# Kernel tuning notes

Hardware: AMD Instinct MI355X
Metric: run time of the kernel (lower is better)

Reference implementation:

```python
import jax, jax.numpy as jnp
import numpy as np

ALPHA = 0.2  # LeakyReLU negative slope
NEG_INF = -9e15


def setup_inputs() -> dict:
    key = jax.random.key(0)
    ks = jax.random.split(key, 6)
    N, IN, OUT, E = 2048, 256, 256, 64
    inp = {
        "input": jax.random.normal(ks[0], (N, IN), dtype=jnp.float32),
        "adj": jax.random.randint(ks[1], (N, N), 0, 2, dtype=jnp.int32),
        "e_feat": jax.random.normal(ks[2], (N, N, E), dtype=jnp.float32),
        # xavier-uniform-like scale for params
        "W_e": jax.random.normal(ks[3], (E, IN), dtype=jnp.float32) * (1.414 * np.sqrt(2.0 / (E + IN))),
        "W": jax.random.normal(ks[4], (IN, OUT), dtype=jnp.float32) * (1.414 * np.sqrt(2.0 / (IN + OUT))),
        "a": jax.random.normal(ks[5], (3 * OUT, 1), dtype=jnp.float32) * (1.414 * np.sqrt(2.0 / (3 * OUT + 1))),
    }
    return inp


def reference(input, adj, e_feat, W_e, W, a):
    F = W.shape[1]
    # Decompose attention vector: cat([h_i, h_j, e_ij]) @ a == h_i@a1 + h_j@a2 + e_ij@a3
    a1, a2, a3 = a[:F, 0], a[F:2 * F, 0], a[2 * F:, 0]
    h = input @ W                              # [N, F]
    s_src = h @ a1                             # [N]
    s_dst = h @ a2                             # [N]
    # e_ij @ a3 where e = e_feat @ W_e @ W, folded by associativity into one [N,N] result
    s_edge = e_feat @ (W_e @ (W @ a3))         # [N, N]
    scores = jax.nn.leaky_relu(s_src[:, None] + s_dst[None, :] + s_edge, negative_slope=ALPHA)
    att = jnp.where(adj > 0, scores, NEG_INF)
    att = jax.nn.softmax(att, axis=1)
    h_prime = att @ h                          # [N, F]
    return jax.nn.elu(h_prime)                 # concat=True -> ELU
```

## Files before the change

kernel.cpp:

```cpp
#include <hip/hip_runtime.h>
#include <math.h>

#define NN   2048
#define INF_ 256
#define OUTF 256
#define EF   64
#define ALPHA 0.2f
#define NEG_INF -9000000000000000.0f

typedef unsigned short ushortT;
typedef __attribute__((ext_vector_type(8))) short    short8v;
typedef __attribute__((ext_vector_type(4))) short    short4v;
typedef __attribute__((ext_vector_type(8))) unsigned short u16x8;
typedef __attribute__((ext_vector_type(4))) float    f32x4;

__device__ __forceinline__ float b2f(ushortT u) {
    unsigned v = (unsigned)u << 16;
    return *(float*)&v;
}
__device__ __forceinline__ ushortT f2b(float f) {
    unsigned b = *(unsigned*)&f;
    unsigned r = (b + 0x7FFFu + ((b >> 16) & 1u)) >> 16;
    return (ushortT)r;
}
__device__ __forceinline__ float dpp_add_xor1(float x) {
    int xi = *(int*)&x;
    int r = __builtin_amdgcn_mov_dpp(xi, 0xB1, 0xF, 0xF, true);
    float rf = *(float*)&r;
    return x + rf;
}
__device__ __forceinline__ float dpp_add_xor2(float x) {
    int xi = *(int*)&x;
    int r = __builtin_amdgcn_mov_dpp(xi, 0x4E, 0xF, 0xF, true);
    float rf = *(float*)&r;
    return x + rf;
}

__global__ void prep1_kernel(const float* __restrict__ W, const float* __restrict__ a,
                             float* __restrict__ w3) {
    int lane = threadIdx.x & 63, wave = threadIdx.x >> 6;
    const float* a3 = a + 2 * OUTF;
    float4 av = *(const float4*)&a3[lane * 4];
    int r0 = blockIdx.x * 8 + wave * 2;
    #pragma unroll
    for (int rr = 0; rr < 2; ++rr) {
        int r = r0 + rr;
        float4 wv = *(const float4*)&W[(size_t)r * OUTF + lane * 4];
        float d = wv.x * av.x + wv.y * av.y + wv.z * av.z + wv.w * av.w;
        #pragma unroll
        for (int off = 32; off; off >>= 1) d += __shfl_xor(d, off);
        if (lane == 0) w3[r] = d;
    }
}

__global__ void prep2_kernel(const float* __restrict__ W_e, const float* __restrict__ w3,
                             float* __restrict__ we3) {
    int lane = threadIdx.x & 63, wave = threadIdx.x >> 6;
    int r = blockIdx.x * 4 + wave;
    float4 wv = *(const float4*)&W_e[(size_t)r * INF_ + lane * 4];
    float4 xv = *(const float4*)&w3[lane * 4];
    float d = wv.x * xv.x + wv.y * xv.y + wv.z * xv.z + wv.w * xv.w;
    #pragma unroll
    for (int off = 32; off; off >>= 1) d += __shfl_xor(d, off);
    if (lane == 0) we3[r] = d;
}

__global__ void sv_kernel(const float* __restrict__ h, const float* __restrict__ a,
                          float* __restrict__ s_src, float* __restrict__ s_dst) {
    int lane = threadIdx.x & 63;
    int wave = threadIdx.x >> 6;
    int i = blockIdx.x * 4 + wave;
    float acc1 = 0.f, acc2 = 0.f;
    #pragma unroll
    for (int u = 0; u < 4; ++u) {
        int o = lane + u * 64;
        float hv = h[(size_t)i * OUTF + o];
        acc1 += hv * a[o];
        acc2 += hv * a[OUTF + o];
    }
    #pragma unroll
    for (int off = 32; off; off >>= 1) {
        acc1 += __shfl_xor(acc1, off);
        acc2 += __shfl_xor(acc2, off);
    }
    if (lane == 0) { s_src[i] = acc1; s_dst[i] = acc2; }
}

template<int K>
__launch_bounds__(256, 2)
__global__ void gemm_kernel(const float* __restrict__ A, const float* __restrict__ Bm,
                            float* __restrict__ C) {
    __shared__ float As[64][68];
    __shared__ float Bs[64][32];
    int tid = threadIdx.x;
    int r0 = blockIdx.x * 64;
    int c0 = blockIdx.y * 32;
    int tr = tid >> 4;
    int tc = tid & 15;
    float acc[4][2] = {};

    for (int k0 = 0; k0 < K; k0 += 64) {
        #pragma unroll
        for (int t = 0; t < 4; ++t) {
            int s = tid + t * 256;
            int row = s >> 4, col4 = s & 15;
            *(float4*)&As[row][col4 * 4] =
                *(const float4*)&A[(size_t)(r0 + row) * K + k0 + col4 * 4];
        }
        #pragma unroll
        for (int t = 0; t < 2; ++t) {
            int s = tid + t * 256;
            int row = s >> 3, col4 = s & 7;
            *(float4*)&Bs[row][col4 * 4] =
                *(const float4*)&Bm[(size_t)(k0 + row) * 256 + c0 + col4 * 4];
        }
        __syncthreads();
        #pragma unroll
        for (int kk = 0; kk < 64; kk += 4) {
            float4 aReg[4];
            float2 bReg[4];
            #pragma unroll
            for (int i = 0; i < 4; ++i) aReg[i] = *(const float4*)&As[tr * 4 + i][kk];
            #pragma unroll
            for (int q = 0; q < 4; ++q)  bReg[q] = *(const float2*)&Bs[kk + q][tc * 2];
            #pragma unroll
            for (int q = 0; q < 4; ++q) {
                float bx = bReg[q].x, by = bReg[q].y;
                #pragma unroll
                for (int i = 0; i < 4; ++i) {
                    float av = (q == 0) ? aReg[i].x : (q == 1) ? aReg[i].y
                             : (q == 2) ? aReg[i].z : aReg[i].w;
                    acc[i][0] += av * bx;
                    acc[i][1] += av * by;
                }
            }
        }
        __syncthreads();
    }
    #pragma unroll
    for (int i = 0; i < 4; ++i) {
        int r = r0 + tr * 4 + i;
        float2 v = {acc[i][0], acc[i][1]};
        *(float2*)&C[(size_t)r * 256 + c0 + tc * 2] = v;
    }
}

__global__ void xpose_kernel(const float* __restrict__ h, ushortT* __restrict__ hbT) {
    __shared__ ushortT tb[64][72];
    int t = threadIdx.x;
    int r0 = blockIdx.x * 64;
    int n0 = blockIdx.y * 64;
    int row = t >> 2, seg = t & 3;
    #pragma unroll
    for (int c = 0; c < 4; ++c) {
        float4 v = *(const float4*)&h[(size_t)(r0 + row) * OUTF + n0 + seg * 16 + c * 4];
        tb[seg * 16 + c * 4 + 0][row] = f2b(v.x);
        tb[seg * 16 + c * 4 + 1][row] = f2b(v.y);
        tb[seg * 16 + c * 4 + 2][row] = f2b(v.z);
        tb[seg * 16 + c * 4 + 3][row] = f2b(v.w);
    }
    __syncthreads();
    *(u16x8*)&hbT[(size_t)(n0 + row) * NN + r0 + seg * 16] =
        *(const u16x8*)&tb[row][seg * 16];
    *(u16x8*)&hbT[(size_t)(n0 + row) * NN + r0 + seg * 16 + 8] =
        *(const u16x8*)&tb[row][seg * 16 + 8];
}

__launch_bounds__(256, 2)
__global__ void gemm2_mfma_kernel(const ushortT* __restrict__ attb,
                                  const ushortT* __restrict__ hbT,
                                  float* __restrict__ Cpart) {
    __shared__ ushortT As[64][72];
    __shared__ ushortT Bs[64][72];
    int tid = threadIdx.x;
    int lane = tid & 63;
    int w = tid >> 6;
    int r0 = blockIdx.x * 64;
    int c0 = blockIdx.y * 64;
    int z  = blockIdx.z;
    int m = lane & 15, q = lane >> 4;
    const int srow = tid >> 2, sseg = tid & 3;

    f32x4 acc0 = {0.f, 0.f, 0.f, 0.f};
    f32x4 acc1 = {0.f, 0.f, 0.f, 0.f};
    f32x4 acc2 = {0.f, 0.f, 0.f, 0.f};
    f32x4 acc3 = {0.f, 0.f, 0.f, 0.f};

    for (int k0 = z * (NN / 4); k0 < (z + 1) * (NN / 4); k0 += 64) {
        {
            const size_t abase = (size_t)(r0 + srow) * NN + k0 + sseg * 16;
            *(u16x8*)&As[srow][sseg * 16]     = *(const u16x8*)&attb[abase];
            *(u16x8*)&As[srow][sseg * 16 + 8] = *(const u16x8*)&attb[abase + 8];
            const size_t bbase = (size_t)(c0 + srow) * NN + k0 + sseg * 16;
            *(u16x8*)&Bs[srow][sseg * 16]     = *(const u16x8*)&hbT[bbase];
            *(u16x8*)&Bs[srow][sseg * 16 + 8] = *(const u16x8*)&hbT[bbase + 8];
        }
        __syncthreads();
        #pragma unroll
        for (int kk = 0; kk < 2; ++kk) {
            short4v a0 = *(const short4v*)&As[w * 16 + m][kk * 32 + q * 4];
            short4v a1 = *(const short4v*)&As[w * 16 + m][kk * 32 + 16 + q * 4];
            short8v af = {a0.x, a0.y, a0.z, a0.w, a1.x, a1.y, a1.z, a1.w};
            #pragma unroll
            for (int nb = 0; nb < 4; ++nb) {
                short4v b0 = *(const short4v*)&Bs[nb * 16 + m][kk * 32 + q * 4];
                short4v b1 = *(const short4v*)&Bs[nb * 16 + m][kk * 32 + 16 + q * 4];
                short8v bf = {b0.x, b0.y, b0.z, b0.w, b1.x, b1.y, b1.z, b1.w};
                if (nb == 0) acc0 = __builtin_amdgcn_mfma_f32_16x16x32_bf16(af, bf, acc0, 0, 0, 0);
                if (nb == 1) acc1 = __builtin_amdgcn_mfma_f32_16x16x32_bf16(af, bf, acc1, 0, 0, 0);
                if (nb == 2) acc2 = __builtin_amdgcn_mfma_f32_16x16x32_bf16(af, bf, acc2, 0, 0, 0);
                if (nb == 3) acc3 = __builtin_amdgcn_mfma_f32_16x16x32_bf16(af, bf, acc3, 0, 0, 0);
            }
        }
        __syncthreads();
    }
    float* Cz = Cpart + (size_t)z * NN * OUTF;
    #pragma unroll
    for (int r = 0; r < 4; ++r) {
        int row = r0 + w * 16 + q * 4 + r;
        Cz[(size_t)row * OUTF + c0 + 0  + m] = acc0[r];
        Cz[(size_t)row * OUTF + c0 + 16 + m] = acc1[r];
        Cz[(size_t)row * OUTF + c0 + 32 + m] = acc2[r];
        Cz[(size_t)row * OUTF + c0 + 48 + m] = acc3[r];
    }
}

__global__ void combine_kernel(const float* __restrict__ Cpart, const float* __restrict__ invs,
                               float* __restrict__ out) {
    int i = blockIdx.x, t = threadIdx.x;
    size_t idx = (size_t)i * OUTF + t;
    const size_t P = (size_t)NN * OUTF;
    float v = (Cpart[idx] + Cpart[P + idx] + Cpart[2 * P + idx] + Cpart[3 * P + idx]) * invs[i];
    out[idx] = v > 0.f ? v : __expf(v) - 1.f;
}

__launch_bounds__(256, 6)
__global__ void score_kernel(const float* __restrict__ e_feat, const int* __restrict__ adj,
                             const float* __restrict__ s_src, const float* __restrict__ s_dst,
                             const float* __restrict__ we3,
                             ushortT* __restrict__ attb, float* __restrict__ invs) {
    __shared__ float p[NN];
    __shared__ float sdst[NN];
    __shared__ unsigned char amask[NN];
    __shared__ float swe3[EF];
    __shared__ float redm[4], reds[4];

    int tid  = threadIdx.x;
    int lane = tid & 63;
    int wave = tid >> 6;
    int i    = blockIdx.x;

    const int* arow = adj + (size_t)i * NN;
    #pragma unroll
    for (int t = 0; t < 2; ++t) {
        int s = tid * 2 + t;
        int4 a4 = ((const int4*)arow)[s];
        uchar4 m4;
        m4.x = a4.x != 0; m4.y = a4.y != 0; m4.z = a4.z != 0; m4.w = a4.w != 0;
        *(uchar4*)&amask[s * 4] = m4;
        ((float4*)sdst)[s] = ((const float4*)s_dst)[s];
    }
    if (tid < EF) swe3[tid] = we3[tid];
    __syncthreads();

    const int g  = lane >> 2;
    const int gl = lane & 3;
    const float4 wv0 = *(const float4*)&swe3[0  + gl * 4];
    const float4 wv1 = *(const float4*)&swe3[16 + gl * 4];
    const float4 wv2 = *(const float4*)&swe3[32 + gl * 4];
    const float4 wv3 = *(const float4*)&swe3[48 + gl * 4];
    const float* efrow = e_feat + (size_t)i * NN * EF;
    const int joff = wave * 16 + g;

    unsigned mbits = 0;
    #pragma unroll
    for (int k = 0; k < 32; ++k)
        mbits |= (unsigned)(amask[k * 64 + joff] != 0) << k;

    #pragma unroll 4
    for (int k = 0; k < 32; ++k) {
        int j = k * 64 + joff;
        bool av = (mbits >> k) & 1u;
        float4 e0, e1, e2, e3;
        if (av) {
            const float* ep = efrow + (size_t)j * EF;
            e0 = *(const float4*)&ep[0  + gl * 4];
            e1 = *(const float4*)&ep[16 + gl * 4];
            e2 = *(const float4*)&ep[32 + gl * 4];
            e3 = *(const float4*)&ep[48 + gl * 4];
        }
        if (av) {
            float d = e0.x * wv0.x + e0.y * wv0.y + e0.z * wv0.z + e0.w * wv0.w
                    + e1.x * wv1.x + e1.y * wv1.y + e1.z * wv1.z + e1.w * wv1.w
                    + e2.x * wv2.x + e2.y * wv2.y + e2.z * wv2.z + e2.w * wv2.w
                    + e3.x * wv3.x + e3.y * wv3.y + e3.z * wv3.z + e3.w * wv3.w;
            d = dpp_add_xor1(d);
            d = dpp_add_xor2(d);
            if (gl == 0) p[j] = d;
        }
    }
    __syncthreads();

    const float ssrc = s_src[i];

    float m = NEG_INF;
    for (int j = tid; j < NN; j += 256) {
        if (amask[j]) {
            float s = ssrc + sdst[j] + p[j];
            s = (s > 0.f) ? s : ALPHA * s;
            m = fmaxf(m, s);
        }
    }
    #pragma unroll
    for (int off = 32; off; off >>= 1) m = fmaxf(m, __shfl_xor(m, off));
    if (lane == 0) redm[wave] = m;
    __syncthreads();
    m = fmaxf(fmaxf(redm[0], redm[1]), fmaxf(redm[2], redm[3]));
    const bool none = (m < -8.0e14f);

    ushortT* arowo = attb + (size_t)i * NN;
    float sum = 0.f;
    for (int j = tid * 2; j < NN; j += 512) {
        float e0, e1;
        if (amask[j]) {
            float s = ssrc + sdst[j] + p[j];
            s = (s > 0.f) ? s : ALPHA * s;
            e0 = __expf(s - m);
        } else e0 = none ? 1.0f : 0.0f;
        if (amask[j + 1]) {
            float s = ssrc + sdst[j + 1] + p[j + 1];
            s = (s > 0.f) ? s : ALPHA * s;
            e1 = __expf(s - m);
        } else e1 = none ? 1.0f : 0.0f;
        ushort2 uu; uu.x = f2b(e0); uu.y = f2b(e1);
        *(ushort2*)&arowo[j] = uu;
        sum += e0 + e1;
    }
    #pragma unroll
    for (int off = 32; off; off >>= 1) sum += __shfl_xor(sum, off);
    if (lane == 0) reds[wave] = sum;
    __syncthreads();
    if (tid == 0) invs[i] = 1.f / (reds[0] + reds[1] + reds[2] + reds[3]);
}

extern "C" void kernel_launch(void* const* d_in, const int* in_sizes, int n_in,
                              void* d_out, int out_size, void* d_ws, size_t ws_size,
                              hipStream_t stream) {
    const float* input  = (const float*)d_in[0];
    const int*   adj    = (const int*)  d_in[1];
    const float* e_feat = (const float*)d_in[2];
    const float* W_e    = (const float*)d_in[3];
    const float* W      = (const float*)d_in[4];
    const float* a      = (const float*)d_in[5];
    float* out = (float*)d_out;

    float*   ws    = (float*)d_ws;
    float*   h     = ws;
    float*   s_src = h + (size_t)NN * OUTF;
    float*   s_dst = s_src + NN;
    float*   w3    = s_dst + NN;
    float*   we3   = w3 + INF_;
    float*   invs  = we3 + EF;
    ushortT* attb  = (ushortT*)(invs + NN);
    ushortT* hbT   = attb + (size_t)NN * NN;
    float*   cpart = (float*)(hbT + (size_t)OUTF * NN);

    prep1_kernel<<<32, 256, 0, stream>>>(W, a, w3);
    prep2_kernel<<<16, 256, 0, stream>>>(W_e, w3, we3);
    gemm_kernel<INF_><<<dim3(NN / 64, 8), 256, 0, stream>>>(input, W, h);
    xpose_kernel<<<dim3(NN / 64, OUTF / 64), 256, 0, stream>>>(h, hbT);
    sv_kernel<<<NN / 4, 256, 0, stream>>>(h, a, s_src, s_dst);
    score_kernel<<<NN, 256, 0, stream>>>(e_feat, adj, s_src, s_dst, we3, attb, invs);
    gemm2_mfma_kernel<<<dim3(NN / 64, OUTF / 64, 4), 256, 0, stream>>>(attb, hbT, cpart);
    combine_kernel<<<NN, 256, 0, stream>>>(cpart, invs, out);
}
```

Baseline: 151.1 us.

## Fuse projection GEMM with transpose and score vectors, drop split-K combine

The input projection GEMM now writes the transposed bf16 h directly and emits per-tile partial s_src/s_dst dot products. This removes the separate fp32 h buffer, the transpose kernel and the score-vector kernel. The prep kernels are merged into one small kernel that also reduces the partials. The aggregation MFMA GEMM drops split-K, using 32x32 tiles over the full K, and applies the softmax normalization and ELU in its epilogue, which eliminates the partial buffer and combine kernel. This trades fewer launches and less memory traffic for smaller per-block tiles and a serial weight-folding block.

```diff
diff --git a/kernel.cpp b/kernel.cpp
--- a/kernel.cpp
+++ b/kernel.cpp
@@ -14,10 +14,6 @@
 typedef __attribute__((ext_vector_type(8))) unsigned short u16x8;
 typedef __attribute__((ext_vector_type(4))) float    f32x4;
 
-__device__ __forceinline__ float b2f(ushortT u) {
-    unsigned v = (unsigned)u << 16;
-    return *(float*)&v;
-}
 __device__ __forceinline__ ushortT f2b(float f) {
     unsigned b = *(unsigned*)&f;
     unsigned r = (b + 0x7FFFu + ((b >> 16) & 1u)) >> 16;
@@ -36,62 +32,14 @@
     return x + rf;
 }
 
-__global__ void prep1_kernel(const float* __restrict__ W, const float* __restrict__ a,
-                             float* __restrict__ w3) {
-    int lane = threadIdx.x & 63, wave = threadIdx.x >> 6;
-    const float* a3 = a + 2 * OUTF;
-    float4 av = *(const float4*)&a3[lane * 4];
-    int r0 = blockIdx.x * 8 + wave * 2;
-    #pragma unroll
-    for (int rr = 0; rr < 2; ++rr) {
-        int r = r0 + rr;
-        float4 wv = *(const float4*)&W[(size_t)r * OUTF + lane * 4];
-        float d = wv.x * av.x + wv.y * av.y + wv.z * av.z + wv.w * av.w;
-        #pragma unroll
-        for (int off = 32; off; off >>= 1) d += __shfl_xor(d, off);
-        if (lane == 0) w3[r] = d;
-    }
-}
-
-__global__ void prep2_kernel(const float* __restrict__ W_e, const float* __restrict__ w3,
-                             float* __restrict__ we3) {
-    int lane = threadIdx.x & 63, wave = threadIdx.x >> 6;
-    int r = blockIdx.x * 4 + wave;
-    float4 wv = *(const float4*)&W_e[(size_t)r * INF_ + lane * 4];
-    float4 xv = *(const float4*)&w3[lane * 4];
-    float d = wv.x * xv.x + wv.y * xv.y + wv.z * xv.z + wv.w * xv.w;
-    #pragma unroll
-    for (int off = 32; off; off >>= 1) d += __shfl_xor(d, off);
-    if (lane == 0) we3[r] = d;
-}
-
-__global__ void sv_kernel(const float* __restrict__ h, const float* __restrict__ a,
-                          float* __restrict__ s_src, float* __restrict__ s_dst) {
-    int lane = threadIdx.x & 63;
-    int wave = threadIdx.x >> 6;
-    int i = blockIdx.x * 4 + wave;
-    float acc1 = 0.f, acc2 = 0.f;
-    #pragma unroll
-    for (int u = 0; u < 4; ++u) {
-        int o = lane + u * 64;
-        float hv = h[(size_t)i * OUTF + o];
-        acc1 += hv * a[o];
-        acc2 += hv * a[OUTF + o];
-    }
-    #pragma unroll
-    for (int off = 32; off; off >>= 1) {
-        acc1 += __shfl_xor(acc1, off);
-        acc2 += __shfl_xor(acc2, off);
-    }
-    if (lane == 0) { s_src[i] = acc1; s_dst[i] = acc2; }
-}
-
-template<int K>
 __launch_bounds__(256, 2)
-__global__ void gemm_kernel(const float* __restrict__ A, const float* __restrict__ Bm,
-                            float* __restrict__ C) {
+__global__ void gemm_fused_kernel(const float* __restrict__ A, const float* __restrict__ Bm,
+                                  const float* __restrict__ a,
+                                  ushortT* __restrict__ hbT, float* __restrict__ psv) {
     __shared__ float As[64][68];
     __shared__ float Bs[64][32];
+    __shared__ ushortT tb[32][72];
+    __shared__ float sp1[64][17], sp2[64][17];
     int tid = threadIdx.x;
     int r0 = blockIdx.x * 64;
     int c0 = blockIdx.y * 32;
@@ -99,13 +47,13 @@
     int tc = tid & 15;
     float acc[4][2] = {};
 
-    for (int k0 = 0; k0 < K; k0 += 64) {
+    for (int k0 = 0; k0 < INF_; k0 += 64) {
         #pragma unroll
         for (int t = 0; t < 4; ++t) {
             int s = tid + t * 256;
             int row = s >> 4, col4 = s & 15;
             *(float4*)&As[row][col4 * 4] =
-                *(const float4*)&A[(size_t)(r0 + row) * K + k0 + col4 * 4];
+                *(const float4*)&A[(size_t)(r0 + row) * INF_ + k0 + col4 * 4];
         }
         #pragma unroll
         for (int t = 0; t < 2; ++t) {
@@ -137,101 +85,70 @@
         }
         __syncthreads();
     }
+
+    const float a1x = a[c0 + tc * 2],        a1y = a[c0 + tc * 2 + 1];
+    const float a2x = a[OUTF + c0 + tc * 2], a2y = a[OUTF + c0 + tc * 2 + 1];
     #pragma unroll
     for (int i = 0; i < 4; ++i) {
-        int r = r0 + tr * 4 + i;
-        float2 v = {acc[i][0], acc[i][1]};
-        *(float2*)&C[(size_t)r * 256 + c0 + tc * 2] = v;
-    }
-}
-
-__global__ void xpose_kernel(const float* __restrict__ h, ushortT* __restrict__ hbT) {
-    __shared__ ushortT tb[64][72];
-    int t = threadIdx.x;
-    int r0 = blockIdx.x * 64;
-    int n0 = blockIdx.y * 64;
-    int row = t >> 2, seg = t & 3;
-    #pragma unroll
-    for (int c = 0; c < 4; ++c) {
-        float4 v = *(const float4*)&h[(size_t)(r0 + row) * OUTF + n0 + seg * 16 + c * 4];
-        tb[seg * 16 + c * 4 + 0][row] = f2b(v.x);
-        tb[seg * 16 + c * 4 + 1][row] = f2b(v.y);
-        tb[seg * 16 + c * 4 + 2][row] = f2b(v.z);
-        tb[seg * 16 + c * 4 + 3][row] = f2b(v.w);
-    }
-    __syncthreads();
-    *(u16x8*)&hbT[(size_t)(n0 + row) * NN + r0 + seg * 16] =
-        *(const u16x8*)&tb[row][seg * 16];
-    *(u16x8*)&hbT[(size_t)(n0 + row) * NN + r0 + seg * 16 + 8] =
-        *(const u16x8*)&tb[row][seg * 16 + 8];
-}
-
-__launch_bounds__(256, 2)
-__global__ void gemm2_mfma_kernel(const ushortT* __restrict__ attb,
-                                  const ushortT* __restrict__ hbT,
-                                  float* __restrict__ Cpart) {
-    __shared__ ushortT As[64][72];
-    __shared__ ushortT Bs[64][72];
-    int tid = threadIdx.x;
-    int lane = tid & 63;
-    int w = tid >> 6;
-    int r0 = blockIdx.x * 64;
-    int c0 = blockIdx.y * 64;
-    int z  = blockIdx.z;
-    int m = lane & 15, q = lane >> 4;
-    const int srow = tid >> 2, sseg = tid & 3;
-
-    f32x4 acc0 = {0.f, 0.f, 0.f, 0.f};
-    f32x4 acc1 = {0.f, 0.f, 0.f, 0.f};
-    f32x4 acc2 = {0.f, 0.f, 0.f, 0.f};
-    f32x4 acc3 = {0.f, 0.f, 0.f, 0.f};
-
-    for (int k0 = z * (NN / 4); k0 < (z + 1) * (NN / 4); k0 += 64) {
-        {
-            const size_t abase = (size_t)(r0 + srow) * NN + k0 + sseg * 16;
-            *(u16x8*)&As[srow][sseg * 16]     = *(const u16x8*)&attb[abase];
-            *(u16x8*)&As[srow][sseg * 16 + 8] = *(const u16x8*)&attb[abase + 8];
-            const size_t bbase = (size_t)(c0 + srow) * NN + k0 + sseg * 16;
-            *(u16x8*)&Bs[srow][sseg * 16]     = *(const u16x8*)&hbT[bbase];
-            *(u16x8*)&Bs[srow][sseg * 16 + 8] = *(const u16x8*)&hbT[bbase + 8];
-        }
-        __syncthreads();
-        #pragma unroll
-        for (int kk = 0; kk < 2; ++kk) {
-            short4v a0 = *(const short4v*)&As[w * 16 + m][kk * 32 + q * 4];
-            short4v a1 = *(const short4v*)&As[w * 16 + m][kk * 32 + 16 + q * 4];
-            short8v af = {a0.x, a0.y, a0.z, a0.w, a1.x, a1.y, a1.z, a1.w};
-            #pragma unroll
-            for (int nb = 0; nb < 4; ++nb) {
-                short4v b0 = *(const short4v*)&Bs[nb * 16 + m][kk * 32 + q * 4];
-                short4v b1 = *(const short4v*)&Bs[nb * 16 + m][kk * 32 + 16 + q * 4];
-                short8v bf = {b0.x, b0.y, b0.z, b0.w, b1.x, b1.y, b1.z, b1.w};
-                if (nb == 0) acc0 = __builtin_amdgcn_mfma_f32_16x16x32_bf16(af, bf, acc0, 0, 0, 0);
-                if (nb == 1) acc1 = __builtin_amdgcn_mfma_f32_16x16x32_bf16(af, bf, acc1, 0, 0, 0);
-                if (nb == 2) acc2 = __builtin_amdgcn_mfma_f32_16x16x32_bf16(af, bf, acc2, 0, 0, 0);
-                if (nb == 3) acc3 = __builtin_amdgcn_mfma_f32_16x16x32_bf16(af, bf, acc3, 0, 0, 0);
-            }
-        }
-        __syncthreads();
-    }
-    float* Cz = Cpart + (size_t)z * NN * OUTF;
-    #pragma unroll
-    for (int r = 0; r < 4; ++r) {
-        int row = r0 + w * 16 + q * 4 + r;
-        Cz[(size_t)row * OUTF + c0 + 0  + m] = acc0[r];
-        Cz[(size_t)row * OUTF + c0 + 16 + m] = acc1[r];
-        Cz[(size_t)row * OUTF + c0 + 32 + m] = acc2[r];
-        Cz[(size_t)row * OUTF + c0 + 48 + m] = acc3[r];
-    }
-}
-
-__global__ void combine_kernel(const float* __restrict__ Cpart, const float* __restrict__ invs,
-                               float* __restrict__ out) {
-    int i = blockIdx.x, t = threadIdx.x;
-    size_t idx = (size_t)i * OUTF + t;
-    const size_t P = (size_t)NN * OUTF;
-    float v = (Cpart[idx] + Cpart[P + idx] + Cpart[2 * P + idx] + Cpart[3 * P + idx]) * invs[i];
-    out[idx] = v > 0.f ? v : __expf(v) - 1.f;
+        int row = tr * 4 + i;
+        tb[tc * 2 + 0][row] = f2b(acc[i][0]);
+        tb[tc * 2 + 1][row] = f2b(acc[i][1]);
+        sp1[row][tc] = acc[i][0] * a1x + acc[i][1] * a1y;
+        sp2[row][tc] = acc[i][0] * a2x + acc[i][1] * a2y;
+    }
+    __syncthreads();
+    {
+        int n = tid >> 3, seg = tid & 7;
+        *(u16x8*)&hbT[(size_t)(c0 + n) * NN + r0 + seg * 8] =
+            *(const u16x8*)&tb[n][seg * 8];
+    }
+    if (tid < 64) {
+        float s1 = 0.f, s2 = 0.f;
+        #pragma unroll
+        for (int c = 0; c < 16; ++c) { s1 += sp1[tid][c]; s2 += sp2[tid][c]; }
+        size_t idx = ((size_t)blockIdx.y * NN + r0 + tid) * 2;
+        psv[idx] = s1; psv[idx + 1] = s2;
+    }
+}
+
+__global__ void svp_kernel(const float* __restrict__ psv, const float* __restrict__ W,
+                           const float* __restrict__ W_e, const float* __restrict__ a,
+                           float* __restrict__ s_src, float* __restrict__ s_dst,
+                           float* __restrict__ we3) {
+    int b = blockIdx.x, tid = threadIdx.x;
+    if (b < 8) {
+        int row = b * 256 + tid;
+        float s1 = 0.f, s2 = 0.f;
+        #pragma unroll
+        for (int ct = 0; ct < 8; ++ct) {
+            size_t idx = ((size_t)ct * NN + row) * 2;
+            s1 += psv[idx]; s2 += psv[idx + 1];
+        }
+        s_src[row] = s1; s_dst[row] = s2;
+        return;
+    }
+    __shared__ float sw3[INF_];
+    int lane = tid & 63, wave = tid >> 6;
+    float4 av = *(const float4*)&a[2 * OUTF + lane * 4];
+    for (int rr = 0; rr < 64; ++rr) {
+        int r = wave * 64 + rr;
+        float4 wv = *(const float4*)&W[(size_t)r * OUTF + lane * 4];
+        float d = wv.x * av.x + wv.y * av.y + wv.z * av.z + wv.w * av.w;
+        #pragma unroll
+        for (int off = 32; off; off >>= 1) d += __shfl_xor(d, off);
+        if (lane == 0) sw3[r] = d;
+    }
+    __syncthreads();
+    float4 xv = *(const float4*)&sw3[lane * 4];
+    #pragma unroll
+    for (int rr = 0; rr < 16; ++rr) {
+        int r = wave * 16 + rr;
+        float4 wv = *(const float4*)&W_e[(size_t)r * INF_ + lane * 4];
+        float d = wv.x * xv.x + wv.y * xv.y + wv.z * xv.z + wv.w * xv.w;
+        #pragma unroll
+        for (int off = 32; off; off >>= 1) d += __shfl_xor(d, off);
+        if (lane == 0) we3[r] = d;
+    }
 }
 
 __launch_bounds__(256, 6)
@@ -343,6 +260,50 @@
     if (tid == 0) invs[i] = 1.f / (reds[0] + reds[1] + reds[2] + reds[3]);
 }
 
+__launch_bounds__(256, 2)
+__global__ void gemm2_mfma_kernel(const ushortT* __restrict__ attb,
+                                  const ushortT* __restrict__ hbT,
+                                  const float* __restrict__ invs,
+                                  float* __restrict__ out) {
+    __shared__ ushortT As[32][72];
+    __shared__ ushortT Bs[32][72];
+    int tid = threadIdx.x;
+    int lane = tid & 63;
+    int w = tid >> 6;
+    int r0 = blockIdx.x * 32;
+    int c0 = blockIdx.y * 32;
+    int m = lane & 15, q = lane >> 4;
+    int mrow = (w & 1) * 16, ncol = (w >> 1) * 16;
+    const int arow = tid >> 3, aseg = tid & 7;
+
+    f32x4 acc = {0.f, 0.f, 0.f, 0.f};
+
+    for (int k0 = 0; k0 < NN; k0 += 64) {
+        *(u16x8*)&As[arow][aseg * 8] =
+            *(const u16x8*)&attb[(size_t)(r0 + arow) * NN + k0 + aseg * 8];
+        *(u16x8*)&Bs[arow][aseg * 8] =
+            *(const u16x8*)&hbT[(size_t)(c0 + arow) * NN + k0 + aseg * 8];
+        __syncthreads();
+        #pragma unroll
+        for (int kk = 0; kk < 2; ++kk) {
+            short4v a0 = *(const short4v*)&As[mrow + m][kk * 32 + q * 4];
+            short4v a1 = *(const short4v*)&As[mrow + m][kk * 32 + 16 + q * 4];
+            short8v af = {a0.x, a0.y, a0.z, a0.w, a1.x, a1.y, a1.z, a1.w};
+            short4v b0 = *(const short4v*)&Bs[ncol + m][kk * 32 + q * 4];
+            short4v b1 = *(const short4v*)&Bs[ncol + m][kk * 32 + 16 + q * 4];
+            short8v bf = {b0.x, b0.y, b0.z, b0.w, b1.x, b1.y, b1.z, b1.w};
+            acc = __builtin_amdgcn_mfma_f32_16x16x32_bf16(af, bf, acc, 0, 0, 0);
+        }
+        __syncthreads();
+    }
+    #pragma unroll
+    for (int r = 0; r < 4; ++r) {
+        int row = r0 + mrow + q * 4 + r;
+        float v = acc[r] * invs[row];
+        out[(size_t)row * OUTF + c0 + ncol + m] = v > 0.f ? v : __expf(v) - 1.f;
+    }
+}
+
 extern "C" void kernel_launch(void* const* d_in, const int* in_sizes, int n_in,
                               void* d_out, int out_size, void* d_ws, size_t ws_size,
                               hipStream_t stream) {
@@ -355,22 +316,16 @@
     float* out = (float*)d_out;
 
     float*   ws    = (float*)d_ws;
-    float*   h     = ws;
-    float*   s_src = h + (size_t)NN * OUTF;
+    float*   psv   = ws;
+    float*   s_src = psv + 8 * NN * 2;
     float*   s_dst = s_src + NN;
-    float*   w3    = s_dst + NN;
-    float*   we3   = w3 + INF_;
+    float*   we3   = s_dst + NN;
     float*   invs  = we3 + EF;
     ushortT* attb  = (ushortT*)(invs + NN);
     ushortT* hbT   = attb + (size_t)NN * NN;
-    float*   cpart = (float*)(hbT + (size_t)OUTF * NN);
-
-    prep1_kernel<<<32, 256, 0, stream>>>(W, a, w3);
-    prep2_kernel<<<16, 256, 0, stream>>>(W_e, w3, we3);
-    gemm_kernel<INF_><<<dim3(NN / 64, 8), 256, 0, stream>>>(input, W, h);
-    xpose_kernel<<<dim3(NN / 64, OUTF / 64), 256, 0, stream>>>(h, hbT);
-    sv_kernel<<<NN / 4, 256, 0, stream>>>(h, a, s_src, s_dst);
+
+    gemm_fused_kernel<<<dim3(NN / 64, 8), 256, 0, stream>>>(input, W, a, hbT, psv);
+    svp_kernel<<<9, 256, 0, stream>>>(psv, W, W_e, a, s_src, s_dst, we3);
     score_kernel<<<NN, 256, 0, stream>>>(e_feat, adj, s_src, s_dst, we3, attb, invs);
-    gemm2_mfma_kernel<<<dim3(NN / 64, OUTF / 64, 4), 256, 0, stream>>>(attb, hbT, cpart);
-    combine_kernel<<<NN, 256, 0, stream>>>(cpart, invs, out);
-}
+    gemm2_mfma_kernel<<<dim3(NN / 32, OUTF / 32), 256, 0, stream>>>(attb, hbT, invs, out);
+}
```

New measurement: 179.1 us. +18.5%, slower.
